# Optimization experiments

Hardware: AMD Instinct MI355X
Metric: run time of the kernel (lower is better)

## Reference

```python
import jax, jax.numpy as jnp
import numpy as np

D_MODEL = 1024
NHEAD = 16
HEAD_DIM = D_MODEL // NHEAD  # 64
THETA = 10000.0


def apply_rope(t):
    # t: [B, H, S, D]. Interleaved-pair RoPE (lucidrains rotary-embedding-torch
    # rotate_queries_or_keys), positions = arange(S), theta = 10000.
    B, H, S, D = t.shape
    inv_freq = 1.0 / (THETA ** (jnp.arange(0, D, 2, dtype=jnp.float32) / D))  # [D/2]
    ang = jnp.arange(S, dtype=jnp.float32)[:, None] * inv_freq               # [S, D/2]
    cos = jnp.cos(ang).astype(t.dtype)
    sin = jnp.sin(ang).astype(t.dtype)
    tp = t.reshape(B, H, S, D // 2, 2)
    x1, x2 = tp[..., 0], tp[..., 1]
    rot = jnp.stack([x1 * cos - x2 * sin, x1 * sin + x2 * cos], axis=-1)
    return rot.reshape(B, H, S, D)


def setup_inputs() -> dict:
    key = jax.random.key(0)
    k0, k1, k2, k3, k4 = jax.random.split(key, 5)
    B, Sx, Sc = 2, 2048, 2048
    sc = 0.02  # weight init scale
    return {
        "x": jax.random.normal(k0, (B, Sx, D_MODEL), jnp.float32),
        "context": jax.random.normal(k1, (B, Sc, D_MODEL), jnp.float32),
        "Wq": jax.random.normal(k2, (D_MODEL, D_MODEL), jnp.float32) * sc,
        "Wv": jax.random.normal(k3, (D_MODEL, D_MODEL), jnp.float32) * sc,
        "Wo": jax.random.normal(k4, (D_MODEL, D_MODEL), jnp.float32) * sc,
        "bo": jnp.zeros((D_MODEL,), jnp.float32),
        "x_pos": jnp.arange(B * Sx, dtype=jnp.int64).reshape(B, Sx) % Sx,
        "context_pos": jnp.arange(B * Sc, dtype=jnp.int64).reshape(B, Sc) % Sc,
    }


def reference(x, context, Wq, Wv, Wo, bo, x_pos, context_pos):
    # x_pos/context_pos are unused when both streams use the internal
    # RotaryEmbedding (is_imu1=is_imu2=True), matching the original forward.
    B, Sx, _ = x.shape
    Sc = context.shape[1]
    q = (x @ Wq.T).reshape(B, Sx, NHEAD, HEAD_DIM).transpose(0, 2, 1, 3)
    # NOTE: original code uses projq (not projk) for keys — replicated here.
    k = (context @ Wq.T).reshape(B, Sc, NHEAD, HEAD_DIM).transpose(0, 2, 1, 3)
    v = (context @ Wv.T).reshape(B, Sc, NHEAD, HEAD_DIM).transpose(0, 2, 1, 3)
    q = apply_rope(q)
    k = apply_rope(k)
    scale = 1.0 / jnp.sqrt(jnp.asarray(HEAD_DIM, q.dtype))
    attn = jax.nn.softmax(jnp.einsum("bhqd,bhkd->bhqk", q, k) * scale, axis=-1)
    out = jnp.einsum("bhqk,bhkd->bhqd", attn, v)            # [B,H,Sx,hd]
    out = out.transpose(0, 2, 1, 3).reshape(B, Sx, D_MODEL)  # [B,Sx,d_model]
    return out @ Wo.T + bo
```

## Files before the change

kernel.cpp:

```cpp
#include <hip/hip_runtime.h>
#include <cmath>


typedef __bf16 bf16x8 __attribute__((ext_vector_type(8)));
typedef __bf16 bf16x4 __attribute__((ext_vector_type(4)));
typedef float f32x4 __attribute__((ext_vector_type(4)));
typedef float f32x16 __attribute__((ext_vector_type(16)));
typedef unsigned u32x4v __attribute__((ext_vector_type(4)));

#define MFMA(A, B, C) __builtin_amdgcn_mfma_f32_16x16x32_bf16(A, B, C, 0, 0, 0)
#define MFMA32(A, B, C) __builtin_amdgcn_mfma_f32_32x32x16_bf16(A, B, C, 0, 0, 0)
#define GLL16(g, l)                                                        \
  __builtin_amdgcn_global_load_lds(                                        \
      (const __attribute__((address_space(1))) unsigned int*)(g),          \
      (__attribute__((address_space(3))) unsigned int*)(l), 16, 0, 0)

#define VMCNT(N) asm volatile("s_waitcnt vmcnt(" #N ")" ::: "memory")
#define BARM() asm volatile("s_barrier" ::: "memory")
#define LGKM0() asm volatile("s_waitcnt lgkmcnt(0)" ::: "memory")

__global__ __launch_bounds__(256) void cvt_all_kernel(
    const float* __restrict__ x, const float* __restrict__ ctx,
    const float* __restrict__ Wq, const float* __restrict__ Wv,
    const float* __restrict__ Wo, __bf16* __restrict__ xb, __bf16* __restrict__ cb,
    __bf16* __restrict__ Wqb, __bf16* __restrict__ Wvb, __bf16* __restrict__ Wob) {
  int base = blockIdx.x * 512 + threadIdx.x;
  const float* src;
  __bf16* dst;
  int off;
  if (base < 1048576) { src = x; dst = xb; off = 0; }
  else if (base < 2097152) { src = ctx; dst = cb; off = 1048576; }
  else if (base < 2359296) { src = Wq; dst = Wqb; off = 2097152; }
  else if (base < 2621440) { src = Wv; dst = Wvb; off = 2359296; }
  else { src = Wo; dst = Wob; off = 2621440; }
#pragma unroll
  for (int jj = 0; jj < 2; jj++) {
    int j = base - off + jj * 256;
    float4 f = ((const float4*)src)[j];
    bf16x4 o;
    o[0] = (__bf16)f.x; o[1] = (__bf16)f.y; o[2] = (__bf16)f.z; o[3] = (__bf16)f.w;
    ((bf16x4*)dst)[j] = o;
  }
}

__global__ __launch_bounds__(512, 2) void gemm_proj(const __bf16* __restrict__ A0,
                                                    const __bf16* __restrict__ W0,
                                                    void* __restrict__ outQ,
                                                    void* __restrict__ outK,
                                                    void* __restrict__ outV) {
  const int tid = threadIdx.x;
  const int wave = tid >> 6, lane = tid & 63, quad = lane >> 4, l15 = lane & 15;
  const int wm = wave >> 2, wn = wave & 3;

  const int id = blockIdx.x;
  int m0, n0;
  const __bf16* A;
  const __bf16* W;
  bool vmode;
  if (id < 128) {
    const int xcd = id & 7, j = id >> 3;
    m0 = (xcd * 4 + (j & 3)) * 256;
    n0 = (j >> 2) * 256;
    A = A0;
    W = W0;
    vmode = false;
  } else {
    const int vid = id - 128;
    const int xcd = vid & 7, j = vid >> 3;
    m0 = (xcd * 2 + (j & 1)) * 256;
    n0 = (j >> 1) * 256;
    A = A0 + (size_t)4096 * 1024;
    W = W0 + (size_t)1024 * 1024;
    vmode = true;
  }

  __shared__ __attribute__((aligned(16))) __bf16 As[2][2][8192];
  __shared__ __attribute__((aligned(16))) __bf16 Bs[2][2][8192];

  const int srow = tid >> 2;
  const int kcg = (tid & 3) ^ (srow & 3);
  const size_t aoff0 = (size_t)srow * 1024 + kcg * 8;
  const size_t aoff1 = (size_t)(srow + 128) * 1024 + kcg * 8;
  const __bf16* Ag = A + (size_t)m0 * 1024;
  const __bf16* Wg = W + (size_t)n0 * 1024;
  const int ldst0 = wave * 512;
  const int ldst1 = 4096 + wave * 512;

  auto stageA = [&](int slot, int kh, int kel) {
    GLL16(Ag + aoff0 + kel, &As[slot][kh][ldst0]);
    GLL16(Ag + aoff1 + kel, &As[slot][kh][ldst1]);
  };
  auto stageB = [&](int slot, int kh, int kel) {
    GLL16(Wg + aoff0 + kel, &Bs[slot][kh][ldst0]);
    GLL16(Wg + aoff1 + kel, &Bs[slot][kh][ldst1]);
  };

  const int xk = (quad ^ (l15 & 3)) * 8;
  int afo[8], bfo[4];
#pragma unroll
  for (int mf = 0; mf < 8; mf++) afo[mf] = (wm * 128 + mf * 16 + l15) * 32 + xk;
#pragma unroll
  for (int nf = 0; nf < 4; nf++) bfo[nf] = (wn * 64 + nf * 16 + l15) * 32 + xk;

  f32x4 acc[8][4] = {};
  bf16x8 bf[4], af[4];

  auto loadB = [&](int slot, int kh) {
#pragma unroll
    for (int nf = 0; nf < 4; nf++) bf[nf] = *(const bf16x8*)&Bs[slot][kh][bfo[nf]];
  };
  auto loadA = [&](int slot, int kh, int mfg) {
#pragma unroll
    for (int mf = 0; mf < 4; mf++)
      af[mf] = *(const bf16x8*)&As[slot][kh][afo[mfg * 4 + mf]];
  };
  auto mfma16 = [&](int mfg) {
    __builtin_amdgcn_s_setprio(1);
#pragma unroll
    for (int mf = 0; mf < 4; mf++)
#pragma unroll
      for (int nf = 0; nf < 4; nf++)
        acc[mfg * 4 + mf][nf] = MFMA(af[mf], bf[nf], acc[mfg * 4 + mf][nf]);
    __builtin_amdgcn_s_setprio(0);
  };

  stageA(0, 0, 0);  stageB(0, 0, 0);
  stageA(0, 1, 32); stageB(0, 1, 32);
  stageA(1, 0, 64); stageB(1, 0, 64);
  VMCNT(8); BARM();

#pragma unroll 1
  for (int j = 0; j < 7; j++) {
    const int kb = j * 128;
    loadB(0, 0); loadA(0, 0, 0); stageA(1, 1, kb + 96);
    BARM(); LGKM0(); mfma16(0); BARM();
    loadA(0, 0, 1); stageB(1, 1, kb + 96);
    BARM(); LGKM0(); mfma16(1); VMCNT(8); BARM();
    loadB(0, 1); loadA(0, 1, 0); stageA(0, 0, kb + 128);
    BARM(); LGKM0(); mfma16(0); BARM();
    loadA(0, 1, 1); stageB(0, 0, kb + 128);
    BARM(); LGKM0(); mfma16(1); VMCNT(8); BARM();
    loadB(1, 0); loadA(1, 0, 0); stageA(0, 1, kb + 160);
    BARM(); LGKM0(); mfma16(0); BARM();
    loadA(1, 0, 1); stageB(0, 1, kb + 160);
    BARM(); LGKM0(); mfma16(1); VMCNT(8); BARM();
    loadB(1, 1); loadA(1, 1, 0); stageA(1, 0, kb + 192);
    BARM(); LGKM0(); mfma16(0); BARM();
    loadA(1, 1, 1); stageB(1, 0, kb + 192);
    BARM(); LGKM0(); mfma16(1); VMCNT(8); BARM();
  }
  {
    loadB(0, 0); loadA(0, 0, 0); stageA(1, 1, 992);
    BARM(); LGKM0(); mfma16(0); BARM();
    loadA(0, 0, 1); stageB(1, 1, 992);
    BARM(); LGKM0(); mfma16(1); VMCNT(8); BARM();
    loadB(0, 1); loadA(0, 1, 0);
    BARM(); LGKM0(); mfma16(0); BARM();
    loadA(0, 1, 1);
    BARM(); LGKM0(); mfma16(1); VMCNT(4); BARM();
    loadB(1, 0); loadA(1, 0, 0);
    BARM(); LGKM0(); mfma16(0); BARM();
    loadA(1, 0, 1);
    BARM(); LGKM0(); mfma16(1); VMCNT(0); BARM();
    loadB(1, 1); loadA(1, 1, 0);
    BARM(); LGKM0(); mfma16(0); BARM();
    loadA(1, 1, 1);
    BARM(); LGKM0(); mfma16(1);
  }

  if (!vmode) {
    const int isK = (m0 >= 4096);
    __bf16* O = (__bf16*)(isK ? outK : outQ);
    const float qsc = isK ? 1.0f : 0.18033688f;
    const int mb = m0 & 4095;
#pragma unroll
    for (int nf = 0; nf < 4; nf++) {
      const int n = n0 + wn * 64 + nf * 16 + l15;
      const int h = n >> 6, d = n & 63, p = d >> 1;
      const float invf_rev =
          __builtin_amdgcn_exp2f(-((float)p * 0.41524101f + 2.6514961f));
#pragma unroll
      for (int mf = 0; mf < 8; mf++) {
#pragma unroll
        for (int r = 0; r < 4; r++) {
          const int row = mb + wm * 128 + mf * 16 + quad * 4 + r;
          const int s = row & 2047, b = row >> 11;
          float v = acc[mf][nf][r];
          float pv = __shfl_xor(v, 1, 64);
          float fr = __builtin_amdgcn_fractf((float)s * invf_rev);
          float sn = __builtin_amdgcn_sinf(fr);
          float cs = __builtin_amdgcn_cosf(fr);
          float res = (lane & 1) ? (pv * sn + v * cs) : (v * cs - pv * sn);
          O[((size_t)(b * 16 + h) * 2048 + s) * 64 + d] = (__bf16)(res * qsc);
        }
      }
    }
  } else {
    __bf16* O = (__bf16*)outV;
#pragma unroll
    for (int nf = 0; nf < 4; nf++) {
      const int n = n0 + wn * 64 + nf * 16 + l15;
      const int h = n >> 6, d = n & 63;
#pragma unroll
      for (int mf = 0; mf < 8; mf++) {
        const int rowb = m0 + wm * 128 + mf * 16 + quad * 4;
        const int s = rowb & 2047, b = rowb >> 11;
        bf16x4 o;
#pragma unroll
        for (int r = 0; r < 4; r++) o[r] = (__bf16)acc[mf][nf][r];
        *(bf16x4*)(O + ((size_t)(b * 16 + h) * 64 + d) * 2048 + s) = o;
      }
    }
  }
}

__global__ __launch_bounds__(256) void gemm_out(const __bf16* __restrict__ A,
                                                const __bf16* __restrict__ W,
                                                float* __restrict__ O,
                                                const float* __restrict__ bias) {
  const int tid = threadIdx.x;
  const int wave = tid >> 6, lane = tid & 63, quad = lane >> 4, l15 = lane & 15;
  const int mw = wave >> 1, nw = wave & 1;
  const int id = blockIdx.x;
  const int xcd = id & 7, j = id >> 3;
  const int m0 = (xcd * 4 + (j & 3)) * 128;
  const int n0 = (j >> 2) * 64;

  __shared__ __attribute__((aligned(16))) __bf16 As[3][4096];
  __shared__ __attribute__((aligned(16))) __bf16 Ws[3][2048];

  int goff[2];
#pragma unroll
  for (int jj = 0; jj < 2; jj++) {
    const int s = jj * 256 + tid;
    const int row = s >> 2;
    const int kcg = (s & 3) ^ ((row >> 1) & 3);
    goff[jj] = row * 1024 + kcg * 8;
  }
  const int wrow = tid >> 2;
  const int wkcg = (tid & 3) ^ ((wrow >> 1) & 3);
  const int goffw = wrow * 1024 + wkcg * 8;

  const __bf16* Ag = A + (size_t)m0 * 1024;
  const __bf16* Wg = W + (size_t)n0 * 1024;
  const int ldsoff0 = wave * 512;
  const int ldsoff1 = 2048 + wave * 512;

  const int sw = (l15 >> 1) & 3;
  int afoff[4], wfoff[2];
#pragma unroll
  for (int t = 0; t < 4; t++)
    afoff[t] = (mw * 64 + t * 16 + l15) * 32 + (quad ^ sw) * 8;
#pragma unroll
  for (int t = 0; t < 2; t++)
    wfoff[t] = (nw * 32 + t * 16 + l15) * 32 + (quad ^ sw) * 8;

  f32x4 acc[4][2] = {};

  auto stage = [&](int buf, int k0) {
    GLL16(Ag + goff[0] + k0, &As[buf][ldsoff0]);
    GLL16(Ag + goff[1] + k0, &As[buf][ldsoff1]);
    GLL16(Wg + goffw + k0, &Ws[buf][ldsoff0]);
  };
  auto compute = [&](int buf) {
    bf16x8 af[4], wf[2];
#pragma unroll
    for (int t = 0; t < 4; t++) af[t] = *(const bf16x8*)&As[buf][afoff[t]];
#pragma unroll
    for (int t = 0; t < 2; t++) wf[t] = *(const bf16x8*)&Ws[buf][wfoff[t]];
#pragma unroll
    for (int mt = 0; mt < 4; mt++)
#pragma unroll
      for (int nt = 0; nt < 2; nt++) acc[mt][nt] = MFMA(af[mt], wf[nt], acc[mt][nt]);
  };

  stage(0, 0);
  stage(1, 32);
  int buf = 0;
  for (int c = 0; c < 32; c++) {
    __syncthreads();
    if (c + 2 < 32) {
      int nb = buf + 2;
      if (nb >= 3) nb -= 3;
      stage(nb, (c + 2) * 32);
    }
    compute(buf);
    buf = (buf == 2) ? 0 : buf + 1;
  }

#pragma unroll
  for (int nt = 0; nt < 2; nt++) {
    const int n = n0 + nw * 32 + nt * 16 + l15;
    const float bv = bias[n];
#pragma unroll
    for (int mt = 0; mt < 4; mt++) {
#pragma unroll
      for (int r = 0; r < 4; r++) {
        const int row = m0 + mw * 64 + mt * 16 + quad * 4 + r;
        O[(size_t)row * 1024 + n] = acc[mt][nt][r] + bv;
      }
    }
  }
}

__global__ __launch_bounds__(512, 4) void attn_kernel(const __bf16* __restrict__ Q,
                                                      const __bf16* __restrict__ K,
                                                      const __bf16* __restrict__ Vt,
                                                      __bf16* __restrict__ Aout) {
  const int tid = threadIdx.x;
  const int wave = tid >> 6, lane = tid & 63;
  const int l31 = lane & 31, hi = lane >> 5;
  const int qg = wave >> 1, kg = wave & 1;
  const int id = blockIdx.x;
  const int j = id >> 3;
  const int bh = ((id & 7) << 2) | (j & 3);
  const int q0 = (j >> 2) << 7;

  const __bf16* Qb = Q + (size_t)bh * (2048 * 64);
  const __bf16* Kb = K + (size_t)bh * (2048 * 64);
  const __bf16* Vb = Vt + (size_t)bh * (64 * 2048);

  __shared__ __attribute__((aligned(16))) __bf16 Kbuf[4][4096];
  __shared__ __attribute__((aligned(16))) __bf16 Vbuf[4][4096];

  bf16x8 qf[4];
  {
    const __bf16* qp = Qb + (size_t)(q0 + qg * 32 + l31) * 64 + hi * 8;
#pragma unroll
    for (int i = 0; i < 4; i++) qf[i] = *(const bf16x8*)(qp + i * 16);
  }

  const __bf16* kgp = Kb + lane * 64 + wave * 8;
  const __bf16* vgp = Vb + (size_t)lane * 2048 + wave * 8;
  const int klds = wave * 512;

  int koff[4];
  {
    const int rk = kg * 32 + l31;
#pragma unroll
    for (int i = 0; i < 4; i++) koff[i] = (2 * i + hi) * 512 + rk * 8;
  }
  int voff[2][2];
#pragma unroll
  for (int dt = 0; dt < 2; dt++) {
    const int rv = dt * 32 + l31;
#pragma unroll
    for (int ks = 0; ks < 2; ks++)
      voff[dt][ks] = (kg * 4 + ks * 2 + hi) * 512 + rv * 8;
  }

  f32x4 rs4 = {};
  f32x16 oacc[2] = {};

  auto stage = [&](int buf, int kt) {
    GLL16(kgp + kt * 64, &Kbuf[buf][klds]);
    GLL16(vgp + kt, &Vbuf[buf][klds]);
  };

  auto compute = [&](int buf) {
    f32x16 s = {};
#pragma unroll
    for (int i = 0; i < 4; i++) {
      bf16x8 kf = *(const bf16x8*)&Kbuf[buf][koff[i]];
      s = MFMA32(kf, qf[i], s);
    }
    float pe[16];
#pragma unroll
    for (int r = 0; r < 16; r++) pe[r] = __builtin_amdgcn_exp2f(s[r]);
#pragma unroll
    for (int r = 0; r < 16; r++) rs4[r & 3] += pe[r];
    bf16x8 pa[2];
#pragma unroll
    for (int sl = 0; sl < 2; sl++) {
      unsigned wa, wb, wc, wd;
      asm("v_cvt_pk_bf16_f32 %0, %1, %2" : "=v"(wa) : "v"(pe[8 * sl + 0]), "v"(pe[8 * sl + 1]));
      asm("v_cvt_pk_bf16_f32 %0, %1, %2" : "=v"(wb) : "v"(pe[8 * sl + 4]), "v"(pe[8 * sl + 5]));
      asm("v_cvt_pk_bf16_f32 %0, %1, %2" : "=v"(wc) : "v"(pe[8 * sl + 2]), "v"(pe[8 * sl + 3]));
      asm("v_cvt_pk_bf16_f32 %0, %1, %2" : "=v"(wd) : "v"(pe[8 * sl + 6]), "v"(pe[8 * sl + 7]));
      asm("v_permlane32_swap_b32 %0, %1" : "+v"(wa), "+v"(wb));
      asm("v_permlane32_swap_b32 %0, %1" : "+v"(wc), "+v"(wd));
      u32x4v t;
      t[0] = wa; t[1] = wc; t[2] = wb; t[3] = wd;
      pa[sl] = __builtin_bit_cast(bf16x8, t);
    }
#pragma unroll
    for (int dt = 0; dt < 2; dt++)
#pragma unroll
      for (int ks = 0; ks < 2; ks++) {
        bf16x8 vf = *(const bf16x8*)&Vbuf[buf][voff[dt][ks]];
        oacc[dt] = MFMA32(pa[ks], vf, oacc[dt]);
      }
  };

  stage(0, 0);
  stage(1, 64);
  for (int kt = 0; kt < 2048; kt += 128) {
    const int p = (kt >> 7) & 1;
    __syncthreads();
    if (kt + 128 < 2048) {
      stage(2 * (p ^ 1), kt + 128);
      stage(2 * (p ^ 1) + 1, kt + 192);
    }
    compute(2 * p);
    compute(2 * p + 1);
  }

  __syncthreads();
  float* Ored = (float*)&Kbuf[0][0];
  float* Lred = (float*)&Vbuf[0][0];

  float lw = (rs4[0] + rs4[1]) + (rs4[2] + rs4[3]);
  lw += __shfl_xor(lw, 32, 64);
  Lred[wave * 64 + lane] = lw;
  if (kg == 1) {
#pragma unroll
    for (int dt = 0; dt < 2; dt++)
#pragma unroll
      for (int r = 0; r < 16; r++)
        Ored[(qg * 32 + dt * 16 + r) * 64 + lane] = oacc[dt][r];
  }
  __syncthreads();
  if (kg == 0) {
    const int b = bh >> 4, h = bh & 15;
#pragma unroll
    for (int r = 0; r < 16; r++) {
      const int qrow = (r & 3) + 8 * (r >> 2) + 4 * hi;
      const float lt =
          Lred[(qg * 2) * 64 + qrow] + Lred[(qg * 2 + 1) * 64 + qrow];
      const float inv = 1.f / lt;
      const int qAbs = q0 + qg * 32 + qrow;
#pragma unroll
      for (int dt = 0; dt < 2; dt++) {
        const float o = oacc[dt][r] + Ored[(qg * 32 + dt * 16 + r) * 64 + lane];
        Aout[((size_t)(b * 2048 + qAbs)) * 1024 + h * 64 + dt * 32 + l31] =
            (__bf16)(o * inv);
      }
    }
  }
}

extern "C" void kernel_launch(void* const* d_in, const int* in_sizes, int n_in,
                              void* d_out, int out_size, void* d_ws, size_t ws_size,
                              hipStream_t stream) {
  const float* x   = (const float*)d_in[0];
  const float* ctx = (const float*)d_in[1];
  const float* Wq  = (const float*)d_in[2];
  const float* Wv  = (const float*)d_in[3];
  const float* Wo  = (const float*)d_in[4];
  const float* bo  = (const float*)d_in[5];

  char* ws = (char*)d_ws;
  const size_t MB = 1024 * 1024;
  __bf16* xb   = (__bf16*)(ws + 0 * MB);
  __bf16* cb   = (__bf16*)(ws + 8 * MB);
  __bf16* Wqb  = (__bf16*)(ws + 16 * MB);
  __bf16* Wvb  = (__bf16*)(ws + 18 * MB);
  __bf16* Wob  = (__bf16*)(ws + 20 * MB);
  __bf16* qh   = (__bf16*)(ws + 22 * MB);
  __bf16* kh   = (__bf16*)(ws + 30 * MB);
  __bf16* vt   = (__bf16*)(ws + 38 * MB);
  __bf16* attn = xb;

  cvt_all_kernel<<<5632, 256, 0, stream>>>(x, ctx, Wq, Wv, Wo, xb, cb, Wqb, Wvb, Wob);

  gemm_proj<<<192, 512, 0, stream>>>(xb, Wqb, (void*)qh, (void*)kh, (void*)vt);

  attn_kernel<<<512, 512, 0, stream>>>(qh, kh, vt, attn);

  gemm_out<<<512, 256, 0, stream>>>(attn, Wob, (float*)d_out, bo);
}
```

Measured before the change: 200.8 us.

## Load V fragments directly from global into registers instead of LDS

```diff
diff --git a/kernel.cpp b/kernel.cpp
--- a/kernel.cpp
+++ b/kernel.cpp
@@ -321,7 +321,7 @@
   const __bf16* Vb = Vt + (size_t)bh * (64 * 2048);
 
   __shared__ __attribute__((aligned(16))) __bf16 Kbuf[4][4096];
-  __shared__ __attribute__((aligned(16))) __bf16 Vbuf[4][4096];
+  __shared__ __attribute__((aligned(16))) float Lred[512];
 
   bf16x8 qf[4];
   {
@@ -331,7 +331,6 @@
   }
 
   const __bf16* kgp = Kb + lane * 64 + wave * 8;
-  const __bf16* vgp = Vb + (size_t)lane * 2048 + wave * 8;
   const int klds = wave * 512;
 
   int koff[4];
@@ -340,24 +339,22 @@
 #pragma unroll
     for (int i = 0; i < 4; i++) koff[i] = (2 * i + hi) * 512 + rk * 8;
   }
-  int voff[2][2];
-#pragma unroll
-  for (int dt = 0; dt < 2; dt++) {
-    const int rv = dt * 32 + l31;
-#pragma unroll
-    for (int ks = 0; ks < 2; ks++)
-      voff[dt][ks] = (kg * 4 + ks * 2 + hi) * 512 + rv * 8;
-  }
+  const __bf16* vgb = Vb + (size_t)l31 * 2048 + (kg * 4 + hi) * 8;
 
   f32x4 rs4 = {};
   f32x16 oacc[2] = {};
 
-  auto stage = [&](int buf, int kt) {
-    GLL16(kgp + kt * 64, &Kbuf[buf][klds]);
-    GLL16(vgp + kt, &Vbuf[buf][klds]);
-  };
-
-  auto compute = [&](int buf) {
+  auto stageK = [&](int buf, int kt) { GLL16(kgp + kt * 64, &Kbuf[buf][klds]); };
+
+  auto loadV = [&](bf16x8 (&vf)[2][2], int ktb) {
+#pragma unroll
+    for (int dt = 0; dt < 2; dt++)
+#pragma unroll
+      for (int ks = 0; ks < 2; ks++)
+        vf[dt][ks] = *(const bf16x8*)(vgb + (size_t)dt * 32 * 2048 + ktb + ks * 16);
+  };
+
+  auto compute = [&](int buf, const bf16x8 (&vf)[2][2]) {
     f32x16 s = {};
 #pragma unroll
     for (int i = 0; i < 4; i++) {
@@ -386,28 +383,29 @@
 #pragma unroll
     for (int dt = 0; dt < 2; dt++)
 #pragma unroll
-      for (int ks = 0; ks < 2; ks++) {
-        bf16x8 vf = *(const bf16x8*)&Vbuf[buf][voff[dt][ks]];
-        oacc[dt] = MFMA32(pa[ks], vf, oacc[dt]);
-      }
-  };
-
-  stage(0, 0);
-  stage(1, 64);
+      for (int ks = 0; ks < 2; ks++)
+        oacc[dt] = MFMA32(pa[ks], vf[dt][ks], oacc[dt]);
+  };
+
+  bf16x8 vX[2][2], vY[2][2];
+  loadV(vX, 0);
+  stageK(0, 0);
+  stageK(1, 64);
   for (int kt = 0; kt < 2048; kt += 128) {
     const int p = (kt >> 7) & 1;
     __syncthreads();
     if (kt + 128 < 2048) {
-      stage(2 * (p ^ 1), kt + 128);
-      stage(2 * (p ^ 1) + 1, kt + 192);
-    }
-    compute(2 * p);
-    compute(2 * p + 1);
+      stageK(2 * (p ^ 1), kt + 128);
+      stageK(2 * (p ^ 1) + 1, kt + 192);
+    }
+    loadV(vY, kt + 64);
+    compute(2 * p, vX);
+    if (kt + 128 < 2048) loadV(vX, kt + 128);
+    compute(2 * p + 1, vY);
   }
 
   __syncthreads();
   float* Ored = (float*)&Kbuf[0][0];
-  float* Lred = (float*)&Vbuf[0][0];
 
   float lw = (rs4[0] + rs4[1]) + (rs4[2] + rs4[3]);
   lw += __shfl_xor(lw, 32, 64);
```

After: 233.3 us. 16.2% more time.
